# Optimization experiments

Measured on AMD Instinct MI355X. Metric: run time of the kernel, lower is better.

## Reference

```python
import jax, jax.numpy as jnp
import numpy as np

B, N = 8, 2048
IN_F, MID1, HID, MID2, OUT_F = 128, 128, 128, 128, 128
BIG = 9e15  # matches torch's 9000000000000000.0 additive mask constant


def _linear_params(key, out_d, in_d):
    # torch Linear layout: W is [out, in]
    kw, kb = jax.random.split(key)
    w = jax.random.normal(kw, (out_d, in_d), jnp.float32) * (1.0 / np.sqrt(in_d))
    b = jax.random.normal(kb, (out_d,), jnp.float32) * 0.01
    return w, b


def setup_inputs() -> dict:
    key = jax.random.key(0)
    ks = jax.random.split(key, 16)
    h = jax.random.normal(ks[0], (B, N, IN_F), jnp.float32)
    adj = jax.random.randint(ks[1], (B, N, N), 0, 2).astype(jnp.float32)
    vae2_fetures = jax.random.normal(ks[2], (B, N, OUT_F), jnp.float32)
    Wv1, bv1 = _linear_params(ks[3], MID1, IN_F)
    Wk1, bk1 = _linear_params(ks[4], MID1, IN_F)
    Wq1, bq1 = _linear_params(ks[5], MID1, IN_F)
    Wo1, bo1 = _linear_params(ks[6], HID, MID1)
    Wv2, bv2 = _linear_params(ks[7], MID2, HID)
    Wk2, bk2 = _linear_params(ks[8], MID2, HID)
    Wq2, bq2 = _linear_params(ks[9], MID2, HID)
    Wo2, bo2 = _linear_params(ks[10], OUT_F, MID2)
    Wf, bf = _linear_params(ks[11], OUT_F, 2 * OUT_F)
    return {
        "h": h, "adj": adj, "vae2_fetures": vae2_fetures,
        "Wv1": Wv1, "bv1": bv1, "Wk1": Wk1, "bk1": bk1, "Wq1": Wq1, "bq1": bq1,
        "Wo1": Wo1, "bo1": bo1,
        "Wv2": Wv2, "bv2": bv2, "Wk2": Wk2, "bk2": bk2, "Wq2": Wq2, "bq2": bq2,
        "Wo2": Wo2, "bo2": bo2, "Wf": Wf, "bf": bf,
    }


def _lin(x, W, b):
    return jnp.einsum('bnd,od->bno', x, W) + b


def _masked_att_block(x, adj, Wq, bq, Wk, bk, Wv, bv):
    v = jax.nn.relu(_lin(x, Wv, bv))          # [B,N,D]
    q = jax.nn.relu(_lin(x, Wq, bq))          # [B,N,D]
    k = jax.nn.relu(_lin(x, Wk, bk))          # [B,N,D]
    s = jnp.einsum('bnd,bmd->bnm', q, k)       # [B,N,N]
    masked = s * adj - BIG * (1.0 - adj)       # multiplicative + additive mask
    att = jax.nn.softmax(masked, axis=-1)
    return jnp.einsum('bnm,bmd->bnd', att, v)


def reference(h, adj, vae2_fetures,
              Wv1, bv1, Wk1, bk1, Wq1, bq1, Wo1, bo1,
              Wv2, bv2, Wk2, bk2, Wq2, bq2, Wo2, bo2,
              Wf, bf):
    f1 = _masked_att_block(h, adj, Wq1, bq1, Wk1, bk1, Wv1, bv1)
    f1 = _lin(f1, Wo1, bo1)                    # [B,N,HID]
    f2 = _masked_att_block(f1, adj, Wq2, bq2, Wk2, bk2, Wv2, bv2)
    f2 = _lin(f2, Wo2, bo2)                    # [B,N,OUT_F]
    f3 = jnp.concatenate([f2, vae2_fetures], axis=2)
    return _lin(f3, Wf, bf)                    # [B,N,OUT_F]
```

## Files before the change

kernel.cpp:

```cpp
#include <hip/hip_runtime.h>

typedef short s16x8 __attribute__((ext_vector_type(8)));
typedef float f32x4 __attribute__((ext_vector_type(4)));
typedef unsigned short u16x4v __attribute__((ext_vector_type(4)));

#define NSPLIT 4
#define NROWS 16384
#define MSHIFT 44.0f

__device__ __forceinline__ unsigned short f2bf(float f) {
  union { float fl; unsigned int i; } v; v.fl = f;
  unsigned int x = v.i;
  x += 0x7fffu + ((x >> 16) & 1u);
  return (unsigned short)(x >> 16);
}
__device__ __forceinline__ s16x8 load8_bf16(const unsigned short* p) {
  return *(const s16x8*)p;
}
__device__ __forceinline__ s16x8 load8_f32(const float* p) {
  float4 a = *(const float4*)p;
  float4 b = *(const float4*)(p + 4);
  s16x8 r;
  r[0] = (short)f2bf(a.x); r[1] = (short)f2bf(a.y);
  r[2] = (short)f2bf(a.z); r[3] = (short)f2bf(a.w);
  r[4] = (short)f2bf(b.x); r[5] = (short)f2bf(b.y);
  r[6] = (short)f2bf(b.z); r[7] = (short)f2bf(b.w);
  return r;
}
__device__ __forceinline__ int vperm(int nn) {
  return (nn & ~31) | (((nn >> 2) & 3) << 3) | (((nn >> 4) & 1) << 2);
}

__device__ __forceinline__ void gload16(const void* g, void* l) {
  __builtin_amdgcn_global_load_lds(
      (const __attribute__((address_space(1))) void*)g,
      (__attribute__((address_space(3))) void*)l, 16, 0, 0);
}

__global__ __launch_bounds__(256) void pack_kernel(
    const float* __restrict__ ADJ, unsigned int* __restrict__ MASK32)
{
  const int t = threadIdx.x;
  const int w = t >> 6;
  const int lane = t & 63;
  const int row0 = blockIdx.x * 32 + w * 8;

  for (int i = 0; i < 8; ++i) {
    const int row = row0 + i;
    const float4* src = (const float4*)(ADJ + (size_t)row * 2048 + lane * 32);
    float4 v[8];
#pragma unroll
    for (int j = 0; j < 8; ++j) v[j] = src[j];

    unsigned int wm = 0u;
#pragma unroll
    for (int j = 0; j < 8; ++j) {
      wm |= (v[j].x != 0.f ? 1u : 0u) << (4 * j);
      wm |= (v[j].y != 0.f ? 2u : 0u) << (4 * j);
      wm |= (v[j].z != 0.f ? 4u : 0u) << (4 * j);
      wm |= (v[j].w != 0.f ? 8u : 0u) << (4 * j);
    }
    MASK32[(size_t)row * 64 + lane] = wm;
  }
}

__global__ __launch_bounds__(256) void gemm_kernel(
    const float* __restrict__ X,
    const float* __restrict__ Wq, const float* __restrict__ bq, unsigned short* __restrict__ oq,
    const float* __restrict__ Wk, const float* __restrict__ bk, unsigned short* __restrict__ ok,
    const float* __restrict__ Wv, const float* __restrict__ bv, unsigned short* __restrict__ ovt)
{
  const int t = threadIdx.x;
  const int w = t >> 6;
  const int lane = t & 63;
  const int l15 = lane & 15;
  const int quad = lane >> 4;
  const int mbase = blockIdx.x * 64;

  s16x8 af[4][4];
#pragma unroll
  for (int mt = 0; mt < 4; ++mt) {
    const float* ar = X + (size_t)(mbase + mt * 16 + l15) * 128;
#pragma unroll
    for (int ks = 0; ks < 4; ++ks) af[mt][ks] = load8_f32(ar + ks * 32 + quad * 8);
  }

  const float* Ws[3] = {Wq, Wk, Wv};
  const float* bs[3] = {bq, bk, bv};
  unsigned short* outs[3] = {oq, ok, ovt};

#pragma unroll
  for (int which = 0; which < 3; ++which) {
    const float* W = Ws[which];
    const float* bias = bs[which];
    unsigned short* out = outs[which];
#pragma unroll
    for (int nt = 0; nt < 2; ++nt) {
      const int n = (w * 2 + nt) * 16 + l15;
      const float* wr = W + (size_t)n * 128;
      s16x8 wf[4];
#pragma unroll
      for (int ks = 0; ks < 4; ++ks) wf[ks] = load8_f32(wr + ks * 32 + quad * 8);
      f32x4 acc[4];
#pragma unroll
      for (int mt = 0; mt < 4; ++mt) acc[mt] = (f32x4){0.f, 0.f, 0.f, 0.f};
#pragma unroll
      for (int mt = 0; mt < 4; ++mt)
#pragma unroll
        for (int ks = 0; ks < 4; ++ks)
          acc[mt] = __builtin_amdgcn_mfma_f32_16x16x32_bf16(af[mt][ks], wf[ks], acc[mt], 0, 0, 0);
      const float bv_ = bias[n];
      if (which < 2) {
#pragma unroll
        for (int mt = 0; mt < 4; ++mt)
#pragma unroll
          for (int r = 0; r < 4; ++r)
            out[(size_t)(mbase + mt * 16 + quad * 4 + r) * 128 + n] =
                f2bf(fmaxf(acc[mt][r] + bv_, 0.f));
      } else {
        const int b = mbase >> 11;
#pragma unroll
        for (int mt = 0; mt < 4; ++mt) {
          const int nn = (mbase & 2047) + mt * 16 + quad * 4;
          u16x4v pk;
#pragma unroll
          for (int r = 0; r < 4; ++r) pk[r] = f2bf(fmaxf(acc[mt][r] + bv_, 0.f));
          *(u16x4v*)(out + (size_t)(b * 128 + n) * 2048 + vperm(nn)) = pk;
        }
      }
    }
  }
}

__global__ __launch_bounds__(256, 2) void attn_kernel(
    const unsigned short* __restrict__ Q,
    const unsigned short* __restrict__ K,
    const unsigned short* __restrict__ VT,
    const unsigned int* __restrict__ MASK32,
    float* __restrict__ pO, float* __restrict__ pl)
{
  __shared__ __align__(16) unsigned short kbuf[2][64][128];
  __shared__ __align__(16) unsigned short vbuf[2][128][64];

  const int t = threadIdx.x;
  const int w = t >> 6;
  const int lane = t & 63;
  const int l15 = lane & 15;
  const int quad = lane >> 4;
  const int x7 = l15 & 7;

  const int gq0 = blockIdx.x * 128;
  const int b   = gq0 >> 11;
  const int wq0 = (gq0 & 2047) + w * 32;
  const int kc0 = blockIdx.y * (2048 / NSPLIT);

  const unsigned short* Kb  = K  + (size_t)(b * 2048) * 128;
  const unsigned short* VTb = VT + (size_t)(b * 128) * 2048;
  const unsigned int* Mb32 = MASK32 + (size_t)b * 2048 * 64;

  const int krow = t >> 4;
  const int kc16 = t & 15;
  const int kchunk = kc16 ^ (krow & 7);
  const int vrow = t >> 3;
  const int vc16 = t & 7;
  const int vchunk = vc16 ^ (vrow & 7);

  s16x8 qf[2][4];
#pragma unroll
  for (int mt = 0; mt < 2; ++mt) {
    const unsigned short* qrow = Q + (size_t)(gq0 + w * 32 + mt * 16 + l15) * 128;
#pragma unroll
    for (int ks = 0; ks < 4; ++ks) qf[mt][ks] = load8_bf16(qrow + ks * 32 + quad * 8);
  }

  s16x8 ones;
#pragma unroll
  for (int i = 0; i < 8; ++i) ones[i] = (short)0x3F80;

  f32x4 accO[2][8];
  f32x4 accL[2];
#pragma unroll
  for (int mt = 0; mt < 2; ++mt) {
    accL[mt] = (f32x4){0.f, 0.f, 0.f, 0.f};
#pragma unroll
    for (int dt = 0; dt < 8; ++dt) accO[mt][dt] = (f32x4){0.f, 0.f, 0.f, 0.f};
  }

#pragma unroll
  for (int i = 0; i < 4; ++i)
    gload16(Kb + (size_t)(kc0 + i * 16 + krow) * 128 + kchunk * 8,
            &kbuf[0][i * 16 + krow][kc16 * 8]);
#pragma unroll
  for (int i = 0; i < 4; ++i)
    gload16(VTb + (size_t)(i * 32 + vrow) * 2048 + kc0 + vchunk * 8,
            &vbuf[0][i * 32 + vrow][vc16 * 8]);

  __syncthreads();

  for (int g = 0; g < 2; ++g) {
    const int jj = (kc0 >> 8) + g;
    uint4 ua[2], ub[2];
#pragma unroll
    for (int mt = 0; mt < 2; ++mt) {
      const unsigned int* mrow =
          Mb32 + (size_t)(wq0 + mt * 16 + l15) * 64 + jj * 8;
      ua[mt] = *(const uint4*)mrow;
      ub[mt] = *(const uint4*)(mrow + 4);
    }

#pragma unroll
    for (int cg = 0; cg < 4; ++cg) {
      const int kc = kc0 + g * 256 + cg * 64;
      unsigned short (*kb)[128] = kbuf[cg & 1];
      unsigned short (*vb)[64]  = vbuf[cg & 1];

      if (g == 0 || cg < 3) {
        unsigned short (*kbn)[128] = kbuf[(cg + 1) & 1];
        unsigned short (*vbn)[64]  = vbuf[(cg + 1) & 1];
#pragma unroll
        for (int i = 0; i < 4; ++i)
          gload16(Kb + (size_t)(kc + 64 + i * 16 + krow) * 128 + kchunk * 8,
                  &kbn[i * 16 + krow][kc16 * 8]);
#pragma unroll
        for (int i = 0; i < 4; ++i)
          gload16(VTb + (size_t)(i * 32 + vrow) * 2048 + (kc + 64) + vchunk * 8,
                  &vbn[i * 32 + vrow][vc16 * 8]);
      }

      f32x4 sv[2][4];
#pragma unroll
      for (int nt = 0; nt < 4; ++nt) {
        sv[0][nt] = (f32x4){0.f, 0.f, 0.f, 0.f};
        sv[1][nt] = (f32x4){0.f, 0.f, 0.f, 0.f};
      }
      __builtin_amdgcn_s_setprio(1);
#pragma unroll
      for (int nt = 0; nt < 4; ++nt)
#pragma unroll
        for (int ks = 0; ks < 4; ++ks) {
          s16x8 kf = *(const s16x8*)&kb[nt * 16 + l15][((ks * 4 + quad) ^ x7) * 8];
          sv[0][nt] = __builtin_amdgcn_mfma_f32_16x16x32_bf16(kf, qf[0][ks], sv[0][nt], 0, 0, 0);
          sv[1][nt] = __builtin_amdgcn_mfma_f32_16x16x32_bf16(kf, qf[1][ks], sv[1][nt], 0, 0, 0);
        }
      __builtin_amdgcn_s_setprio(0);

      s16x8 pf[2][2];
#pragma unroll
      for (int mt = 0; mt < 2; ++mt) {
        const unsigned int wA = (cg == 0) ? ua[mt].x : (cg == 1) ? ua[mt].z
                               : (cg == 2) ? ub[mt].x : ub[mt].z;
        const unsigned int wB = (cg == 0) ? ua[mt].y : (cg == 1) ? ua[mt].w
                               : (cg == 2) ? ub[mt].y : ub[mt].w;
        const unsigned int bA = wA >> (quad * 4);
        const unsigned int bB = wB >> (quad * 4);
#pragma unroll
        for (int ks = 0; ks < 2; ++ks) {
          const unsigned int bits = (ks == 0) ? bA : bB;
          s16x8 v;
#pragma unroll
          for (int half = 0; half < 2; ++half) {
            const int nt = ks * 2 + half;
#pragma unroll
            for (int r = 0; r < 4; ++r) {
              const float e = __expf(sv[mt][nt][r] - MSHIFT);
              const bool keep = (bits >> (half * 16 + r)) & 1u;
              v[half * 4 + r] = (short)f2bf(keep ? e : 0.f);
            }
          }
          pf[mt][ks] = v;
        }
      }

      __builtin_amdgcn_s_setprio(1);
#pragma unroll
      for (int mt = 0; mt < 2; ++mt)
#pragma unroll
        for (int ks = 0; ks < 2; ++ks)
          accL[mt] = __builtin_amdgcn_mfma_f32_16x16x32_bf16(ones, pf[mt][ks], accL[mt], 0, 0, 0);

#pragma unroll
      for (int dt = 0; dt < 8; ++dt)
#pragma unroll
        for (int ks = 0; ks < 2; ++ks) {
          s16x8 vf = *(const s16x8*)&vb[dt * 16 + l15][((ks * 4 + quad) ^ x7) * 8];
          accO[0][dt] = __builtin_amdgcn_mfma_f32_16x16x32_bf16(vf, pf[0][ks], accO[0][dt], 0, 0, 0);
          accO[1][dt] = __builtin_amdgcn_mfma_f32_16x16x32_bf16(vf, pf[1][ks], accO[1][dt], 0, 0, 0);
        }
      __builtin_amdgcn_s_setprio(0);

      __syncthreads();
    }
  }

  float* pOs = pO + (size_t)blockIdx.y * NROWS * 128;
#pragma unroll
  for (int mt = 0; mt < 2; ++mt) {
    const int qg = gq0 + w * 32 + mt * 16 + l15;
#pragma unroll
    for (int dt = 0; dt < 8; ++dt)
      *(f32x4*)(pOs + (size_t)qg * 128 + dt * 16 + quad * 4) = accO[mt][dt];
  }
  if (quad == 0) {
#pragma unroll
    for (int mt = 0; mt < 2; ++mt)
      pl[blockIdx.y * NROWS + gq0 + w * 32 + mt * 16 + l15] = accL[mt][0];
  }
}

__device__ __forceinline__ void combine64(
    const float* __restrict__ pO, const float* __restrict__ pl, int grow0,
    unsigned short (*At)[136])
{
  const int t = threadIdx.x;
#pragma unroll
  for (int u = 0; u < 4; ++u) {
    const int unit = u * 256 + t;
    const int row = unit >> 4;
    const int col8 = (unit & 15) * 8;
    const int grow = grow0 + row;
    float lsum = 0.f;
#pragma unroll
    for (int s = 0; s < NSPLIT; ++s) lsum += pl[s * NROWS + grow];
    const float inv = (lsum > 0.f) ? 1.f / lsum : 0.f;
    float acc8[8];
#pragma unroll
    for (int i = 0; i < 8; ++i) acc8[i] = 0.f;
#pragma unroll
    for (int s = 0; s < NSPLIT; ++s) {
      const float* p = pO + (size_t)s * NROWS * 128 + (size_t)grow * 128 + col8;
      float4 x0 = *(const float4*)p;
      float4 x1 = *(const float4*)(p + 4);
      acc8[0] += x0.x; acc8[1] += x0.y; acc8[2] += x0.z; acc8[3] += x0.w;
      acc8[4] += x1.x; acc8[5] += x1.y; acc8[6] += x1.z; acc8[7] += x1.w;
    }
#pragma unroll
    for (int i = 0; i < 8; ++i) At[row][col8 + i] = f2bf(acc8[i] * inv);
  }
}

__global__ __launch_bounds__(256) void redqkv_kernel(
    const float* __restrict__ pO, const float* __restrict__ pl,
    const float* __restrict__ Wo, const float* __restrict__ bo,
    const float* __restrict__ Wq, const float* __restrict__ bq, unsigned short* __restrict__ oq,
    const float* __restrict__ Wk, const float* __restrict__ bk, unsigned short* __restrict__ ok,
    const float* __restrict__ Wv, const float* __restrict__ bv, unsigned short* __restrict__ ovt)
{
  __shared__ __align__(16) unsigned short At[64][136];
  __shared__ __align__(16) unsigned short Bt[64][136];
  const int t = threadIdx.x;
  const int grow0 = blockIdx.x * 64;

  combine64(pO, pl, grow0, At);
  __syncthreads();

  const int w = t >> 6;
  const int lane = t & 63;
  const int l15 = lane & 15;
  const int quad = lane >> 4;

  s16x8 af[4][4];
#pragma unroll
  for (int mt = 0; mt < 4; ++mt)
#pragma unroll
    for (int ks = 0; ks < 4; ++ks)
      af[mt][ks] = *(const s16x8*)&At[mt * 16 + l15][ks * 32 + quad * 8];

#pragma unroll
  for (int nt = 0; nt < 2; ++nt) {
    const int n = (w * 2 + nt) * 16 + l15;
    const float* wr = Wo + (size_t)n * 128;
    s16x8 wf[4];
#pragma unroll
    for (int ks = 0; ks < 4; ++ks) wf[ks] = load8_f32(wr + ks * 32 + quad * 8);
    f32x4 acc[4];
#pragma unroll
    for (int mt = 0; mt < 4; ++mt) acc[mt] = (f32x4){0.f, 0.f, 0.f, 0.f};
#pragma unroll
    for (int mt = 0; mt < 4; ++mt)
#pragma unroll
      for (int ks = 0; ks < 4; ++ks)
        acc[mt] = __builtin_amdgcn_mfma_f32_16x16x32_bf16(af[mt][ks], wf[ks], acc[mt], 0, 0, 0);
    const float bv_ = bo[n];
#pragma unroll
    for (int mt = 0; mt < 4; ++mt)
#pragma unroll
      for (int r = 0; r < 4; ++r)
        Bt[mt * 16 + quad * 4 + r][n] = f2bf(acc[mt][r] + bv_);
  }
  __syncthreads();

  s16x8 a2[4][4];
#pragma unroll
  for (int mt = 0; mt < 4; ++mt)
#pragma unroll
    for (int ks = 0; ks < 4; ++ks)
      a2[mt][ks] = *(const s16x8*)&Bt[mt * 16 + l15][ks * 32 + quad * 8];

#pragma unroll
  for (int which = 0; which < 3; ++which) {
    const float* W = (which == 0) ? Wq : (which == 1) ? Wk : Wv;
    const float* bb = (which == 0) ? bq : (which == 1) ? bk : bv;
    unsigned short* out = (which == 0) ? oq : (which == 1) ? ok : ovt;
#pragma unroll
    for (int nt = 0; nt < 2; ++nt) {
      const int n = (w * 2 + nt) * 16 + l15;
      const float* wr = W + (size_t)n * 128;
      s16x8 wf[4];
#pragma unroll
      for (int ks = 0; ks < 4; ++ks) wf[ks] = load8_f32(wr + ks * 32 + quad * 8);
      f32x4 acc[4];
#pragma unroll
      for (int mt = 0; mt < 4; ++mt) acc[mt] = (f32x4){0.f, 0.f, 0.f, 0.f};
#pragma unroll
      for (int mt = 0; mt < 4; ++mt)
#pragma unroll
        for (int ks = 0; ks < 4; ++ks)
          acc[mt] = __builtin_amdgcn_mfma_f32_16x16x32_bf16(a2[mt][ks], wf[ks], acc[mt], 0, 0, 0);
      const float bv_ = bb[n];
      if (which < 2) {
#pragma unroll
        for (int mt = 0; mt < 4; ++mt)
#pragma unroll
          for (int r = 0; r < 4; ++r)
            out[(size_t)(grow0 + mt * 16 + quad * 4 + r) * 128 + n] =
                f2bf(fmaxf(acc[mt][r] + bv_, 0.f));
      } else {
        const int b = grow0 >> 11;
#pragma unroll
        for (int mt = 0; mt < 4; ++mt) {
          const int nn = (grow0 & 2047) + mt * 16 + quad * 4;
          u16x4v pk;
#pragma unroll
          for (int r = 0; r < 4; ++r) pk[r] = f2bf(fmaxf(acc[mt][r] + bv_, 0.f));
          *(u16x4v*)(out + (size_t)(b * 128 + n) * 2048 + vperm(nn)) = pk;
        }
      }
    }
  }
}

__global__ __launch_bounds__(256) void redfinal_kernel(
    const float* __restrict__ pO, const float* __restrict__ pl,
    const float* __restrict__ Wo, const float* __restrict__ bo,
    const float* __restrict__ Wf, const float* __restrict__ bff,
    const float* __restrict__ vae2, float* __restrict__ out)
{
  __shared__ __align__(16) unsigned short At[64][136];
  __shared__ __align__(16) unsigned short Bt[64][136];
  const int t = threadIdx.x;
  const int grow0 = blockIdx.x * 64;

  combine64(pO, pl, grow0, At);
  __syncthreads();

  const int w = t >> 6;
  const int lane = t & 63;
  const int l15 = lane & 15;
  const int quad = lane >> 4;

  s16x8 af[4][4];
#pragma unroll
  for (int mt = 0; mt < 4; ++mt)
#pragma unroll
    for (int ks = 0; ks < 4; ++ks)
      af[mt][ks] = *(const s16x8*)&At[mt * 16 + l15][ks * 32 + quad * 8];

#pragma unroll
  for (int nt = 0; nt < 2; ++nt) {
    const int n = (w * 2 + nt) * 16 + l15;
    const float* wr = Wo + (size_t)n * 128;
    s16x8 wf[4];
#pragma unroll
    for (int ks = 0; ks < 4; ++ks) wf[ks] = load8_f32(wr + ks * 32 + quad * 8);
    f32x4 acc[4];
#pragma unroll
    for (int mt = 0; mt < 4; ++mt) acc[mt] = (f32x4){0.f, 0.f, 0.f, 0.f};
#pragma unroll
    for (int mt = 0; mt < 4; ++mt)
#pragma unroll
      for (int ks = 0; ks < 4; ++ks)
        acc[mt] = __builtin_amdgcn_mfma_f32_16x16x32_bf16(af[mt][ks], wf[ks], acc[mt], 0, 0, 0);
    const float bv_ = bo[n];
#pragma unroll
    for (int mt = 0; mt < 4; ++mt)
#pragma unroll
      for (int r = 0; r < 4; ++r)
        Bt[mt * 16 + quad * 4 + r][n] = f2bf(acc[mt][r] + bv_);
  }
  __syncthreads();

  s16x8 a1[4][4], a2[4][4];
#pragma unroll
  for (int mt = 0; mt < 4; ++mt) {
#pragma unroll
    for (int ks = 0; ks < 4; ++ks)
      a1[mt][ks] = *(const s16x8*)&Bt[mt * 16 + l15][ks * 32 + quad * 8];
    const float* vrow = vae2 + (size_t)(grow0 + mt * 16 + l15) * 128;
#pragma unroll
    for (int ks = 0; ks < 4; ++ks) a2[mt][ks] = load8_f32(vrow + ks * 32 + quad * 8);
  }

#pragma unroll
  for (int nt = 0; nt < 2; ++nt) {
    const int n = (w * 2 + nt) * 16 + l15;
    const float* wr = Wf + (size_t)n * 256;
    s16x8 wfl[4], wfr[4];
#pragma unroll
    for (int ks = 0; ks < 4; ++ks) {
      wfl[ks] = load8_f32(wr + ks * 32 + quad * 8);
      wfr[ks] = load8_f32(wr + 128 + ks * 32 + quad * 8);
    }
    f32x4 acc[4];
#pragma unroll
    for (int mt = 0; mt < 4; ++mt) acc[mt] = (f32x4){0.f, 0.f, 0.f, 0.f};
#pragma unroll
    for (int mt = 0; mt < 4; ++mt) {
#pragma unroll
      for (int ks = 0; ks < 4; ++ks)
        acc[mt] = __builtin_amdgcn_mfma_f32_16x16x32_bf16(a1[mt][ks], wfl[ks], acc[mt], 0, 0, 0);
#pragma unroll
      for (int ks = 0; ks < 4; ++ks)
        acc[mt] = __builtin_amdgcn_mfma_f32_16x16x32_bf16(a2[mt][ks], wfr[ks], acc[mt], 0, 0, 0);
    }
    const float bv_ = bff[n];
#pragma unroll
    for (int mt = 0; mt < 4; ++mt)
#pragma unroll
      for (int r = 0; r < 4; ++r)
        out[(size_t)(grow0 + mt * 16 + quad * 4 + r) * 128 + n] = acc[mt][r] + bv_;
  }
}

extern "C" void kernel_launch(void* const* d_in, const int* in_sizes, int n_in,
                              void* d_out, int out_size, void* d_ws, size_t ws_size,
                              hipStream_t stream)
{
  const float* h    = (const float*)d_in[0];
  const float* adj  = (const float*)d_in[1];
  const float* vae2 = (const float*)d_in[2];
  const float* Wv1  = (const float*)d_in[3];
  const float* bv1  = (const float*)d_in[4];
  const float* Wk1  = (const float*)d_in[5];
  const float* bk1  = (const float*)d_in[6];
  const float* Wq1  = (const float*)d_in[7];
  const float* bq1  = (const float*)d_in[8];
  const float* Wo1  = (const float*)d_in[9];
  const float* bo1  = (const float*)d_in[10];
  const float* Wv2  = (const float*)d_in[11];
  const float* bv2  = (const float*)d_in[12];
  const float* Wk2  = (const float*)d_in[13];
  const float* bk2  = (const float*)d_in[14];
  const float* Wq2  = (const float*)d_in[15];
  const float* bq2  = (const float*)d_in[16];
  const float* Wo2  = (const float*)d_in[17];
  const float* bo2  = (const float*)d_in[18];
  const float* Wf   = (const float*)d_in[19];
  const float* bff  = (const float*)d_in[20];

  char* wsb = (char*)d_ws;
  const size_t MB = 1u << 20;
  unsigned short* s_q  = (unsigned short*)(wsb + 0 * MB);
  unsigned short* s_k  = (unsigned short*)(wsb + 4 * MB);
  unsigned short* s_vt = (unsigned short*)(wsb + 8 * MB);
  unsigned int* maskp  = (unsigned int*)(wsb + 12 * MB);
  float* pO = (float*)(wsb + 16 * MB);
  float* pl = (float*)(wsb + 48 * MB);

  gemm_kernel<<<dim3(256), dim3(256), 0, stream>>>(
      h, Wq1, bq1, s_q, Wk1, bk1, s_k, Wv1, bv1, s_vt);
  pack_kernel<<<dim3(512), dim3(256), 0, stream>>>(adj, maskp);
  attn_kernel<<<dim3(128, NSPLIT), dim3(256), 0, stream>>>(
      s_q, s_k, s_vt, maskp, pO, pl);
  redqkv_kernel<<<dim3(256), dim3(256), 0, stream>>>(
      pO, pl, Wo1, bo1, Wq2, bq2, s_q, Wk2, bk2, s_k, Wv2, bv2, s_vt);
  attn_kernel<<<dim3(128, NSPLIT), dim3(256), 0, stream>>>(
      s_q, s_k, s_vt, maskp, pO, pl);
  redfinal_kernel<<<dim3(256), dim3(256), 0, stream>>>(
      pO, pl, Wo2, bo2, Wf, bff, vae2, (float*)d_out);
}
```

Baseline: 343.6 us.

## Halve attention tile sizes to raise block count and occupancy

The attention kernel now gives each wave 16 query rows instead of 32 and streams keys in 32-wide chunks instead of 64. This halves LDS buffers and register accumulators, doubles the grid to 256x4 blocks, and raises the launch-bounds occupancy hint from 2 to 3 blocks per CU. The aim is better latency hiding and fuller use of the GPU's CUs. In exchange, each K/V tile loaded to LDS is reused by fewer query rows, so global/LDS traffic per FLOP roughly doubles, and there are twice as many loop iterations with __syncthreads barriers.

New measurement: 344.0 us. Within noise of the previous version (+0.1%).

```diff
diff --git a/kernel.cpp b/kernel.cpp
--- a/kernel.cpp
+++ b/kernel.cpp
@@ -132,15 +132,15 @@
   }
 }
 
-__global__ __launch_bounds__(256, 2) void attn_kernel(
+__global__ __launch_bounds__(256, 3) void attn_kernel(
     const unsigned short* __restrict__ Q,
     const unsigned short* __restrict__ K,
     const unsigned short* __restrict__ VT,
     const unsigned int* __restrict__ MASK32,
     float* __restrict__ pO, float* __restrict__ pl)
 {
-  __shared__ __align__(16) unsigned short kbuf[2][64][128];
-  __shared__ __align__(16) unsigned short vbuf[2][128][64];
+  __shared__ __align__(16) unsigned short kbuf[2][32][128];
+  __shared__ __align__(16) unsigned short vbuf[2][128][32];
 
   const int t = threadIdx.x;
   const int w = t >> 6;
@@ -148,144 +148,119 @@
   const int l15 = lane & 15;
   const int quad = lane >> 4;
   const int x7 = l15 & 7;
-
-  const int gq0 = blockIdx.x * 128;
+  const int x3 = l15 & 3;
+
+  const int gq0 = blockIdx.x * 64;
   const int b   = gq0 >> 11;
-  const int wq0 = (gq0 & 2047) + w * 32;
+  const int wq0 = (gq0 & 2047) + w * 16;
   const int kc0 = blockIdx.y * (2048 / NSPLIT);
 
   const unsigned short* Kb  = K  + (size_t)(b * 2048) * 128;
   const unsigned short* VTb = VT + (size_t)(b * 128) * 2048;
   const unsigned int* Mb32 = MASK32 + (size_t)b * 2048 * 64;
 
-  const int krow = t >> 4;
-  const int kc16 = t & 15;
-  const int kchunk = kc16 ^ (krow & 7);
-  const int vrow = t >> 3;
-  const int vc16 = t & 7;
-  const int vchunk = vc16 ^ (vrow & 7);
-
-  s16x8 qf[2][4];
-#pragma unroll
-  for (int mt = 0; mt < 2; ++mt) {
-    const unsigned short* qrow = Q + (size_t)(gq0 + w * 32 + mt * 16 + l15) * 128;
-#pragma unroll
-    for (int ks = 0; ks < 4; ++ks) qf[mt][ks] = load8_bf16(qrow + ks * 32 + quad * 8);
+  const int kchunk = (t & 15) ^ ((t >> 4) & 7);
+  const int vchunk = (t & 3) ^ ((t >> 2) & 3);
+
+  s16x8 qf[4];
+  {
+    const unsigned short* qrow = Q + (size_t)(gq0 + w * 16 + l15) * 128;
+#pragma unroll
+    for (int ks = 0; ks < 4; ++ks) qf[ks] = load8_bf16(qrow + ks * 32 + quad * 8);
   }
 
   s16x8 ones;
 #pragma unroll
   for (int i = 0; i < 8; ++i) ones[i] = (short)0x3F80;
 
-  f32x4 accO[2][8];
-  f32x4 accL[2];
-#pragma unroll
-  for (int mt = 0; mt < 2; ++mt) {
-    accL[mt] = (f32x4){0.f, 0.f, 0.f, 0.f};
-#pragma unroll
-    for (int dt = 0; dt < 8; ++dt) accO[mt][dt] = (f32x4){0.f, 0.f, 0.f, 0.f};
-  }
-
-#pragma unroll
-  for (int i = 0; i < 4; ++i)
-    gload16(Kb + (size_t)(kc0 + i * 16 + krow) * 128 + kchunk * 8,
-            &kbuf[0][i * 16 + krow][kc16 * 8]);
-#pragma unroll
-  for (int i = 0; i < 4; ++i)
-    gload16(VTb + (size_t)(i * 32 + vrow) * 2048 + kc0 + vchunk * 8,
-            &vbuf[0][i * 32 + vrow][vc16 * 8]);
+  f32x4 accO[8];
+  f32x4 accL = (f32x4){0.f, 0.f, 0.f, 0.f};
+#pragma unroll
+  for (int dt = 0; dt < 8; ++dt) accO[dt] = (f32x4){0.f, 0.f, 0.f, 0.f};
+
+#pragma unroll
+  for (int i = 0; i < 2; ++i) {
+    const int slot = i * 256 + t;
+    gload16(Kb + (size_t)(kc0 + (slot >> 4)) * 128 + kchunk * 8,
+            &kbuf[0][slot >> 4][(slot & 15) * 8]);
+  }
+#pragma unroll
+  for (int i = 0; i < 2; ++i) {
+    const int slot = i * 256 + t;
+    gload16(VTb + (size_t)(slot >> 2) * 2048 + kc0 + vchunk * 8,
+            &vbuf[0][slot >> 2][(slot & 3) * 8]);
+  }
 
   __syncthreads();
 
   for (int g = 0; g < 2; ++g) {
     const int jj = (kc0 >> 8) + g;
-    uint4 ua[2], ub[2];
-#pragma unroll
-    for (int mt = 0; mt < 2; ++mt) {
-      const unsigned int* mrow =
-          Mb32 + (size_t)(wq0 + mt * 16 + l15) * 64 + jj * 8;
-      ua[mt] = *(const uint4*)mrow;
-      ub[mt] = *(const uint4*)(mrow + 4);
-    }
-
-#pragma unroll
-    for (int cg = 0; cg < 4; ++cg) {
-      const int kc = kc0 + g * 256 + cg * 64;
+    uint4 ua, ub;
+    {
+      const unsigned int* mrow = Mb32 + (size_t)(wq0 + l15) * 64 + jj * 8;
+      ua = *(const uint4*)mrow;
+      ub = *(const uint4*)(mrow + 4);
+    }
+
+#pragma unroll
+    for (int cg = 0; cg < 8; ++cg) {
+      const int kc = kc0 + g * 256 + cg * 32;
       unsigned short (*kb)[128] = kbuf[cg & 1];
-      unsigned short (*vb)[64]  = vbuf[cg & 1];
-
-      if (g == 0 || cg < 3) {
+      unsigned short (*vb)[32]  = vbuf[cg & 1];
+
+      if (g == 0 || cg < 7) {
         unsigned short (*kbn)[128] = kbuf[(cg + 1) & 1];
-        unsigned short (*vbn)[64]  = vbuf[(cg + 1) & 1];
-#pragma unroll
-        for (int i = 0; i < 4; ++i)
-          gload16(Kb + (size_t)(kc + 64 + i * 16 + krow) * 128 + kchunk * 8,
-                  &kbn[i * 16 + krow][kc16 * 8]);
-#pragma unroll
-        for (int i = 0; i < 4; ++i)
-          gload16(VTb + (size_t)(i * 32 + vrow) * 2048 + (kc + 64) + vchunk * 8,
-                  &vbn[i * 32 + vrow][vc16 * 8]);
+        unsigned short (*vbn)[32]  = vbuf[(cg + 1) & 1];
+#pragma unroll
+        for (int i = 0; i < 2; ++i) {
+          const int slot = i * 256 + t;
+          gload16(Kb + (size_t)(kc + 32 + (slot >> 4)) * 128 + kchunk * 8,
+                  &kbn[slot >> 4][(slot & 15) * 8]);
+        }
+#pragma unroll
+        for (int i = 0; i < 2; ++i) {
+          const int slot = i * 256 + t;
+          gload16(VTb + (size_t)(slot >> 2) * 2048 + (kc + 32) + vchunk * 8,
+                  &vbn[slot >> 2][(slot & 3) * 8]);
+        }
       }
 
-      f32x4 sv[2][4];
-#pragma unroll
-      for (int nt = 0; nt < 4; ++nt) {
-        sv[0][nt] = (f32x4){0.f, 0.f, 0.f, 0.f};
-        sv[1][nt] = (f32x4){0.f, 0.f, 0.f, 0.f};
-      }
+      f32x4 sv[2];
+      sv[0] = (f32x4){0.f, 0.f, 0.f, 0.f};
+      sv[1] = (f32x4){0.f, 0.f, 0.f, 0.f};
       __builtin_amdgcn_s_setprio(1);
 #pragma unroll
-      for (int nt = 0; nt < 4; ++nt)
+      for (int nt = 0; nt < 2; ++nt)
 #pragma unroll
         for (int ks = 0; ks < 4; ++ks) {
           s16x8 kf = *(const s16x8*)&kb[nt * 16 + l15][((ks * 4 + quad) ^ x7) * 8];
-          sv[0][nt] = __builtin_amdgcn_mfma_f32_16x16x32_bf16(kf, qf[0][ks], sv[0][nt], 0, 0, 0);
-          sv[1][nt] = __builtin_amdgcn_mfma_f32_16x16x32_bf16(kf, qf[1][ks], sv[1][nt], 0, 0, 0);
+          sv[nt] = __builtin_amdgcn_mfma_f32_16x16x32_bf16(kf, qf[ks], sv[nt], 0, 0, 0);
         }
       __builtin_amdgcn_s_setprio(0);
 
-      s16x8 pf[2][2];
-#pragma unroll
-      for (int mt = 0; mt < 2; ++mt) {
-        const unsigned int wA = (cg == 0) ? ua[mt].x : (cg == 1) ? ua[mt].z
-                               : (cg == 2) ? ub[mt].x : ub[mt].z;
-        const unsigned int wB = (cg == 0) ? ua[mt].y : (cg == 1) ? ua[mt].w
-                               : (cg == 2) ? ub[mt].y : ub[mt].w;
-        const unsigned int bA = wA >> (quad * 4);
-        const unsigned int bB = wB >> (quad * 4);
-#pragma unroll
-        for (int ks = 0; ks < 2; ++ks) {
-          const unsigned int bits = (ks == 0) ? bA : bB;
-          s16x8 v;
-#pragma unroll
-          for (int half = 0; half < 2; ++half) {
-            const int nt = ks * 2 + half;
-#pragma unroll
-            for (int r = 0; r < 4; ++r) {
-              const float e = __expf(sv[mt][nt][r] - MSHIFT);
-              const bool keep = (bits >> (half * 16 + r)) & 1u;
-              v[half * 4 + r] = (short)f2bf(keep ? e : 0.f);
-            }
-          }
-          pf[mt][ks] = v;
+      const unsigned int word = (cg == 0) ? ua.x : (cg == 1) ? ua.y
+                               : (cg == 2) ? ua.z : (cg == 3) ? ua.w
+                               : (cg == 4) ? ub.x : (cg == 5) ? ub.y
+                               : (cg == 6) ? ub.z : ub.w;
+      const unsigned int bits = word >> (quad * 4);
+      s16x8 pf;
+#pragma unroll
+      for (int nt = 0; nt < 2; ++nt)
+#pragma unroll
+        for (int r = 0; r < 4; ++r) {
+          const float e = __expf(sv[nt][r] - MSHIFT);
+          const bool keep = (bits >> (nt * 16 + r)) & 1u;
+          pf[nt * 4 + r] = (short)f2bf(keep ? e : 0.f);
         }
+
+      __builtin_amdgcn_s_setprio(1);
+      accL = __builtin_amdgcn_mfma_f32_16x16x32_bf16(ones, pf, accL, 0, 0, 0);
+
+#pragma unroll
+      for (int dt = 0; dt < 8; ++dt) {
+        s16x8 vf = *(const s16x8*)&vb[dt * 16 + l15][(quad ^ x3) * 8];
+        accO[dt] = __builtin_amdgcn_mfma_f32_16x16x32_bf16(vf, pf, accO[dt], 0, 0, 0);
       }
-
-      __builtin_amdgcn_s_setprio(1);
-#pragma unroll
-      for (int mt = 0; mt < 2; ++mt)
-#pragma unroll
-        for (int ks = 0; ks < 2; ++ks)
-          accL[mt] = __builtin_amdgcn_mfma_f32_16x16x32_bf16(ones, pf[mt][ks], accL[mt], 0, 0, 0);
-
-#pragma unroll
-      for (int dt = 0; dt < 8; ++dt)
-#pragma unroll
-        for (int ks = 0; ks < 2; ++ks) {
-          s16x8 vf = *(const s16x8*)&vb[dt * 16 + l15][((ks * 4 + quad) ^ x7) * 8];
-          accO[0][dt] = __builtin_amdgcn_mfma_f32_16x16x32_bf16(vf, pf[0][ks], accO[0][dt], 0, 0, 0);
-          accO[1][dt] = __builtin_amdgcn_mfma_f32_16x16x32_bf16(vf, pf[1][ks], accO[1][dt], 0, 0, 0);
-        }
       __builtin_amdgcn_s_setprio(0);
 
       __syncthreads();
@@ -293,17 +268,12 @@
   }
 
   float* pOs = pO + (size_t)blockIdx.y * NROWS * 128;
-#pragma unroll
-  for (int mt = 0; mt < 2; ++mt) {
-    const int qg = gq0 + w * 32 + mt * 16 + l15;
+  {
+    const int qg = gq0 + w * 16 + l15;
 #pragma unroll
     for (int dt = 0; dt < 8; ++dt)
-      *(f32x4*)(pOs + (size_t)qg * 128 + dt * 16 + quad * 4) = accO[mt][dt];
-  }
-  if (quad == 0) {
-#pragma unroll
-    for (int mt = 0; mt < 2; ++mt)
-      pl[blockIdx.y * NROWS + gq0 + w * 32 + mt * 16 + l15] = accL[mt][0];
+      *(f32x4*)(pOs + (size_t)qg * 128 + dt * 16 + quad * 4) = accO[dt];
+    if (quad == 0) pl[blockIdx.y * NROWS + qg] = accL[0];
   }
 }
 
@@ -569,11 +539,11 @@
   gemm_kernel<<<dim3(256), dim3(256), 0, stream>>>(
       h, Wq1, bq1, s_q, Wk1, bk1, s_k, Wv1, bv1, s_vt);
   pack_kernel<<<dim3(512), dim3(256), 0, stream>>>(adj, maskp);
-  attn_kernel<<<dim3(128, NSPLIT), dim3(256), 0, stream>>>(
+  attn_kernel<<<dim3(256, NSPLIT), dim3(256), 0, stream>>>(
       s_q, s_k, s_vt, maskp, pO, pl);
   redqkv_kernel<<<dim3(256), dim3(256), 0, stream>>>(
       pO, pl, Wo1, bo1, Wq2, bq2, s_q, Wk2, bk2, s_k, Wv2, bv2, s_vt);
-  attn_kernel<<<dim3(128, NSPLIT), dim3(256), 0, stream>>>(
+  attn_kernel<<<dim3(256, NSPLIT), dim3(256), 0, stream>>>(
       s_q, s_k, s_vt, maskp, pO, pl);
   redfinal_kernel<<<dim3(256), dim3(256), 0, stream>>>(
       pO, pl, Wo2, bo2, Wf, bff, vae2, (float*)d_out);
```
